# Optimization experiments

Hardware: AMD Instinct MI355X
Metric: run time of the kernel (lower is better)

Reference implementation:

```python
import jax, jax.numpy as jnp
import numpy as np

ALPHA, BETA, GAMMA = 67.0, 3.0, 1.0  # DenseCRFParams3d defaults
NUM_ITERATIONS = 5


def _gauss_kernel(feats):
    # feats: (F, N) scaled features; returns (N, N) kernel exp(-0.5*||f_i-f_j||^2)
    sq = jnp.sum(feats * feats, axis=0)
    d2 = sq[:, None] + sq[None, :] - 2.0 * (feats.T @ feats)
    return jnp.exp(-0.5 * jnp.maximum(d2, 0.0))


def _filter(K, q_ln):
    # K: (N, N) symmetric Gaussian kernel; q_ln: (L, N)
    # normalized Gaussian filtering (splat/blur/slice with slice normalization)
    out = q_ln @ K  # (L, N); K symmetric
    norm = jnp.sum(K, axis=0)  # K @ ones
    return out / norm[None, :]


def setup_inputs() -> dict:
    key = jax.random.key(0)
    k1, k2 = jax.random.split(key)
    L, C, D, W, H = 21, 3, 16, 16, 16
    image = jax.random.uniform(k1, (1, C, D, W, H), dtype=jnp.float32)
    logits = jax.random.normal(k2, (1, L, D, W, H), dtype=jnp.float32)
    spatial_ker_weights = 3.0 * jnp.eye(L, dtype=jnp.float32)
    bilateral_ker_weights = 5.0 * jnp.eye(L, dtype=jnp.float32)
    compatibility_matrix = jnp.eye(L, dtype=jnp.float32)
    return {
        "image": image,
        "logits": logits,
        "spatial_ker_weights": spatial_ker_weights,
        "bilateral_ker_weights": bilateral_ker_weights,
        "compatibility_matrix": compatibility_matrix,
    }


def reference(image, logits, spatial_ker_weights, bilateral_ker_weights, compatibility_matrix):
    img = image[0]            # (C, D, W, H)
    unary = logits[0]         # (L, D, W, H)
    C, D, W, H = img.shape
    L = unary.shape[0]
    N = D * W * H

    # voxel coordinates (3, N)
    zz, yy, xx = jnp.meshgrid(jnp.arange(D), jnp.arange(W), jnp.arange(H), indexing="ij")
    pos = jnp.stack([zz, yy, xx]).reshape(3, N).astype(jnp.float32)

    # kernels are fixed across iterations -> build once
    K_sp = _gauss_kernel(pos / GAMMA)                                   # spatial kernel
    feats_bi = jnp.concatenate([pos / ALPHA, img.reshape(C, N) / BETA], axis=0)
    K_bi = _gauss_kernel(feats_bi)                                      # bilateral kernel

    cur = unary
    for _ in range(NUM_ITERATIONS):
        q = jax.nn.softmax(cur, axis=0).reshape(L, N)
        spatial_out = spatial_ker_weights @ _filter(K_sp, q)
        bilateral_out = bilateral_ker_weights @ _filter(K_bi, q)
        msg = compatibility_matrix @ (spatial_out + bilateral_out)
        cur = msg.reshape(L, D, W, H) + unary
    return cur[None]  # (1, L, D, W, H)
```

## Files before the change

kernel.cpp:

```cpp
#include <hip/hip_runtime.h>

#define L 21
#define NVOX 4096
#define ITERS 5
#define NU 210
#define UPAD 224
#define VPB 16
#define NSPLIT 16
#define USPL 14

__global__ __launch_bounds__(256) void phase_ab(
    const float* __restrict__ img, const float* __restrict__ logits,
    const float* __restrict__ Wsp, const float* __restrict__ Wbi,
    const float* __restrict__ Wc,
    float* __restrict__ Phi, float* __restrict__ nsp, float* __restrict__ q,
    float* __restrict__ cu, float* __restrict__ W1, float* __restrict__ W2,
    float* __restrict__ A2)
{
    const int tid = threadIdx.x;
    const int bid = blockIdx.x;
    if (bid < 64) {
        int lane = tid & 63, w = tid >> 6;
        int i = bid * 64 + lane;
        int z = i >> 8, yy = (i >> 4) & 15, xx = i & 15;
        const float ia = 1.0f / 67.0f, ib = 1.0f / 3.0f;
        float f[6];
        f[0] = (float)z * ia; f[1] = (float)yy * ia; f[2] = (float)xx * ia;
        f[3] = img[i] * ib; f[4] = img[NVOX + i] * ib; f[5] = img[2 * NVOX + i] * ib;
        float p[6][5];
#pragma unroll
        for (int c = 0; c < 6; c++) {
            p[c][0] = 1.f;
#pragma unroll
            for (int k = 1; k < 5; k++) p[c][k] = p[c][k - 1] * f[c];
        }
        float hsv = 0.5f * (f[0]*f[0] + f[1]*f[1] + f[2]*f[2] +
                            f[3]*f[3] + f[4]*f[4] + f[5]*f[5]);
        float e0 = __expf(-hsv);
        int ulo = w * 56, uhi = ulo + 56;
        int u = 0;
        for (int a0 = 0; a0 <= 4; a0++)
        for (int a1 = 0; a1 <= 4 - a0; a1++)
        for (int a2 = 0; a2 <= 4 - a0 - a1; a2++)
        for (int a3 = 0; a3 <= 4 - a0 - a1 - a2; a3++)
        for (int a4 = 0; a4 <= 4 - a0 - a1 - a2 - a3; a4++)
        for (int a5 = 0; a5 <= 4 - a0 - a1 - a2 - a3 - a4; a5++) {
            if (u >= ulo && u < uhi)
                Phi[(size_t)u * NVOX + i] =
                    e0 * p[0][a0] * p[1][a1] * p[2][a2] * p[3][a3] * p[4][a4] * p[5][a5];
            u++;
        }
        if (w == 3)
            for (int uz = NU; uz < UPAD; uz++) Phi[(size_t)uz * NVOX + i] = 0.f;
        if (w == 0) {
            float hz = 0.f, hy = 0.f, hx = 0.f;
            for (int t = 0; t < 16; t++) {
                float dz = (float)(z - t), dy = (float)(yy - t), dx = (float)(xx - t);
                hz += __expf(-0.5f * dz * dz);
                hy += __expf(-0.5f * dy * dy);
                hx += __expf(-0.5f * dx * dx);
            }
            nsp[i] = hz * hy * hx;
        }
        if (w == 1) {
            float vals[L]; float mx = -1e30f;
#pragma unroll
            for (int l = 0; l < L; l++) { vals[l] = logits[l * NVOX + i]; mx = fmaxf(mx, vals[l]); }
            float sum = 0.f;
#pragma unroll
            for (int l = 0; l < L; l++) { vals[l] = __expf(vals[l] - mx); sum += vals[l]; }
            float inv = 1.f / sum;
#pragma unroll
            for (int l = 0; l < L; l++) q[l * NVOX + i] = vals[l] * inv;
        }
    } else if (bid == 64) {
        for (int e = tid; e < L * L; e += 256) {
            int r = e / L, c = e % L;
            float s1 = 0.f, s2 = 0.f;
            for (int k = 0; k < L; k++) {
                float wc = Wc[r * L + k];
                s1 = fmaf(wc, Wsp[k * L + c], s1);
                s2 = fmaf(wc, Wbi[k * L + c], s2);
            }
            W1[e] = s1; W2[e] = s2;
        }
    } else if (bid == 65) {
        const float invf[5] = {1.f, 1.f, 0.5f, 1.f / 6.f, 1.f / 24.f};
        float mine = 0.f;
        int v = 0;
        for (int a0 = 0; a0 <= 4; a0++)
        for (int a1 = 0; a1 <= 4 - a0; a1++)
        for (int a2 = 0; a2 <= 4 - a0 - a1; a2++)
        for (int a3 = 0; a3 <= 4 - a0 - a1 - a2; a3++)
        for (int a4 = 0; a4 <= 4 - a0 - a1 - a2 - a3; a4++)
        for (int a5 = 0; a5 <= 4 - a0 - a1 - a2 - a3 - a4; a5++) {
            if (v == tid)
                mine = invf[a0] * invf[a1] * invf[a2] * invf[a3] * invf[a4] * invf[a5];
            v++;
        }
        cu[tid] = mine;
    } else {
        for (int e = tid; e < 2 * 22 * UPAD; e += 256) A2[e] = 0.f;
    }
}

__global__ __launch_bounds__(1024) void phase_p2(
    const float* __restrict__ Phi, const float* __restrict__ q,
    const float* __restrict__ cu, const float* __restrict__ W2,
    float* __restrict__ A2cur, float* __restrict__ spv)
{
    __shared__ float buf[NVOX];
    __shared__ float tmp[NVOX];
    __shared__ float g[16];
    const int tid = threadIdx.x;
    const int bid = blockIdx.x;
    if (bid < NU) {
        int lane = tid & 63, w = tid >> 4 >> 2;
        int i0 = w * 256;
        float4 p = ((const float4*)(Phi + (size_t)bid * NVOX + i0))[lane];
        float acc[22];
        acc[21] = p.x + p.y + p.z + p.w;
#pragma unroll
        for (int m = 0; m < L; m++) {
            float4 qv = ((const float4*)(q + m * NVOX + i0))[lane];
            acc[m] = fmaf(qv.x, p.x, fmaf(qv.y, p.y,
                     fmaf(qv.z, p.z, qv.w * p.w)));
        }
#pragma unroll
        for (int off = 32; off >= 1; off >>= 1)
#pragma unroll
            for (int m = 0; m < 22; m++)
                acc[m] += __shfl_xor(acc[m], off);
        if (lane < 22) {
            float val;
            if (lane < L) {
                float dot = 0.f;
#pragma unroll
                for (int m = 0; m < L; m++)
                    dot = fmaf(W2[lane * L + m], acc[m], dot);
                val = cu[bid] * dot;
            } else {
                val = cu[bid] * acc[21];
            }
            atomicAdd(&A2cur[lane * UPAD + bid], val);
        }
    } else {
        int l = bid - NU;
        if (tid < 16) g[tid] = __expf(-0.5f * (float)(tid * tid));
        for (int k = 0; k < 4; k++)
            buf[tid + 1024 * k] = q[l * NVOX + tid + 1024 * k];
        __syncthreads();
        for (int k = 0; k < 4; k++) {
            int idx = tid + 1024 * k;
            int x = idx & 15, base = idx & ~15;
            float ssum = 0.f;
#pragma unroll
            for (int t = 0; t < 16; t++) {
                int d = x - t; d = d < 0 ? -d : d;
                ssum += g[d] * buf[base + t];
            }
            tmp[idx] = ssum;
        }
        __syncthreads();
        for (int k = 0; k < 4; k++) {
            int idx = tid + 1024 * k;
            int y = (idx >> 4) & 15, base = idx & ~(15 << 4);
            float ssum = 0.f;
#pragma unroll
            for (int t = 0; t < 16; t++) {
                int d = y - t; d = d < 0 ? -d : d;
                ssum += g[d] * tmp[base + (t << 4)];
            }
            buf[idx] = ssum;
        }
        __syncthreads();
        for (int k = 0; k < 4; k++) {
            int idx = tid + 1024 * k;
            int z = idx >> 8, base = idx & 255;
            float ssum = 0.f;
#pragma unroll
            for (int t = 0; t < 16; t++) {
                int d = z - t; d = d < 0 ? -d : d;
                ssum += g[d] * buf[base + (t << 8)];
            }
            spv[l * NVOX + idx] = ssum;
        }
    }
}

__global__ __launch_bounds__(256) void phase_p3(
    const float* __restrict__ Phi, const float* __restrict__ A2cur,
    float* __restrict__ A2next, const float* __restrict__ spv,
    const float* __restrict__ nsp, const float* __restrict__ W1,
    const float* __restrict__ logits, float* __restrict__ q,
    float* __restrict__ out, int last)
{
    __shared__ float sA[L * UPAD];
    __shared__ float sN[UPAD];
    __shared__ float red[22][NSPLIT][VPB];
    __shared__ float sw1[L * L];
    __shared__ float sspn[VPB][22];
    __shared__ float scur[VPB][22];
    const int tid = threadIdx.x;
    const int bid = blockIdx.x;
    const int v = tid & (VPB - 1);
    const int s = tid >> 4;
    const int i16 = bid * VPB + v;

    {
        int e = bid * 256 + tid;
        if (e < 22 * UPAD) A2next[e] = 0.f;
    }
    for (int e = tid; e < L * UPAD; e += 256) sA[e] = A2cur[e];
    for (int e = tid; e < UPAD; e += 256) sN[e] = A2cur[L * UPAD + e];
    for (int e = tid; e < L * L; e += 256) sw1[e] = W1[e];
    {
        float rsp = 1.f / nsp[i16];
        for (int m = s; m < L; m += NSPLIT)
            sspn[v][m] = spv[m * NVOX + i16] * rsp;
    }
    __syncthreads();
    float acc[L], accN = 0.f;
#pragma unroll
    for (int m = 0; m < L; m++) acc[m] = 0.f;
    int u0 = s * USPL;
    for (int uu = 0; uu < USPL; uu++) {
        float p = Phi[(size_t)(u0 + uu) * NVOX + i16];
#pragma unroll
        for (int m = 0; m < L; m++)
            acc[m] = fmaf(sA[m * UPAD + u0 + uu], p, acc[m]);
        accN = fmaf(sN[u0 + uu], p, accN);
    }
#pragma unroll
    for (int m = 0; m < L; m++) red[m][s][v] = acc[m];
    red[21][s][v] = accN;
    __syncthreads();
    float b21 = 0.f;
#pragma unroll
    for (int ss = 0; ss < NSPLIT; ss++) b21 += red[21][ss][v];
    float rbi = 1.f / b21;
    for (int l = s; l < L; l += NSPLIT) {
        float bl = 0.f;
#pragma unroll
        for (int ss = 0; ss < NSPLIT; ss++) bl += red[l][ss][v];
        float r = bl * rbi;
#pragma unroll
        for (int m = 0; m < L; m++)
            r = fmaf(sw1[l * L + m], sspn[v][m], r);
        r += logits[l * NVOX + i16];
        scur[v][l] = r;
        if (last) out[l * NVOX + i16] = r;
    }
    __syncthreads();
    if (!last && tid < VPB) {
        int i = bid * VPB + tid;
        float vals[L]; float mx = -1e30f;
#pragma unroll
        for (int l = 0; l < L; l++) { vals[l] = scur[tid][l]; mx = fmaxf(mx, vals[l]); }
        float sum = 0.f;
#pragma unroll
        for (int l = 0; l < L; l++) { vals[l] = __expf(vals[l] - mx); sum += vals[l]; }
        float inv = 1.f / sum;
#pragma unroll
        for (int l = 0; l < L; l++) q[l * NVOX + i] = vals[l] * inv;
    }
}

extern "C" void kernel_launch(void* const* d_in, const int* in_sizes, int n_in,
                              void* d_out, int out_size, void* d_ws, size_t ws_size,
                              hipStream_t stream) {
    const float* image  = (const float*)d_in[0];
    const float* logits = (const float*)d_in[1];
    const float* Wsp    = (const float*)d_in[2];
    const float* Wbi    = (const float*)d_in[3];
    const float* Wc     = (const float*)d_in[4];
    float* out = (float*)d_out;

    char* ws = (char*)d_ws;
    float* Phi   = (float*)ws; ws += (size_t)UPAD * NVOX * sizeof(float);
    float* nsp   = (float*)ws; ws += (size_t)NVOX * sizeof(float);
    float* q     = (float*)ws; ws += (size_t)L * NVOX * sizeof(float);
    float* spv   = (float*)ws; ws += (size_t)L * NVOX * sizeof(float);
    float* A2    = (float*)ws; ws += (size_t)2 * 22 * UPAD * sizeof(float);
    float* cu    = (float*)ws; ws += (size_t)256 * sizeof(float);
    float* W1    = (float*)ws; ws += (size_t)L * L * sizeof(float);
    float* W2    = (float*)ws; ws += (size_t)L * L * sizeof(float);

    phase_ab<<<67, 256, 0, stream>>>(image, logits, Wsp, Wbi, Wc,
                                     Phi, nsp, q, cu, W1, W2, A2);
    for (int it = 0; it < ITERS; it++) {
        float* A2cur  = A2 + (it & 1) * 22 * UPAD;
        float* A2next = A2 + ((it + 1) & 1) * 22 * UPAD;
        phase_p2<<<NU + L, 1024, 0, stream>>>(Phi, q, cu, W2, A2cur, spv);
        phase_p3<<<256, 256, 0, stream>>>(Phi, A2cur, A2next, spv, nsp,
                                          W1, logits, q, out,
                                          it == ITERS - 1 ? 1 : 0);
    }
}
```

Measured before the change: 160.8 us.

## Process four feature rows per block and truncate spatial blur to radius four

The projection phase now assigns four feature rows to each block, with each wave covering 1024 voxels over four float4 steps. This cuts the grid from 210 to 56 projection blocks and reduces shuffle reductions and atomics per row. The separable spatial blur drops taps beyond distance four and uses constant weights in registers instead of shared memory, which changes results slightly (dropped weights are below about 4e-6). Shared-memory staging of A2 in phase_p3 is switched to float4 loads.

```diff
diff --git a/kernel.cpp b/kernel.cpp
--- a/kernel.cpp
+++ b/kernel.cpp
@@ -8,6 +8,7 @@
 #define VPB 16
 #define NSPLIT 16
 #define USPL 14
+#define NG1B 56
 
 __global__ __launch_bounds__(256) void phase_ab(
     const float* __restrict__ img, const float* __restrict__ logits,
@@ -111,20 +112,29 @@
 {
     __shared__ float buf[NVOX];
     __shared__ float tmp[NVOX];
-    __shared__ float g[16];
     const int tid = threadIdx.x;
     const int bid = blockIdx.x;
-    if (bid < NU) {
-        int lane = tid & 63, w = tid >> 4 >> 2;
-        int i0 = w * 256;
-        float4 p = ((const float4*)(Phi + (size_t)bid * NVOX + i0))[lane];
+    const float garr[5] = {1.0f, 0.60653066f, 0.13533528f,
+                           0.011108997f, 3.3546263e-4f};
+    if (bid < NG1B) {
+        const int lane = tid & 63, wv = tid >> 6;
+        const int u = bid * 4 + (wv >> 2);
+        const int i0 = (wv & 3) * 1024;
         float acc[22];
-        acc[21] = p.x + p.y + p.z + p.w;
-#pragma unroll
-        for (int m = 0; m < L; m++) {
-            float4 qv = ((const float4*)(q + m * NVOX + i0))[lane];
-            acc[m] = fmaf(qv.x, p.x, fmaf(qv.y, p.y,
-                     fmaf(qv.z, p.z, qv.w * p.w)));
+#pragma unroll
+        for (int m = 0; m < 22; m++) acc[m] = 0.f;
+        const float4* ph = (const float4*)(Phi + (size_t)u * NVOX + i0);
+#pragma unroll
+        for (int rep = 0; rep < 4; rep++) {
+            int ii = rep * 64 + lane;
+            float4 pv = ph[ii];
+            acc[21] += pv.x + pv.y + pv.z + pv.w;
+#pragma unroll
+            for (int m = 0; m < L; m++) {
+                float4 qv = ((const float4*)(q + m * NVOX + i0))[ii];
+                acc[m] = fmaf(qv.x, pv.x, fmaf(qv.y, pv.y,
+                         fmaf(qv.z, pv.z, fmaf(qv.w, pv.w, acc[m]))));
+            }
         }
 #pragma unroll
         for (int off = 32; off >= 1; off >>= 1)
@@ -138,15 +148,14 @@
 #pragma unroll
                 for (int m = 0; m < L; m++)
                     dot = fmaf(W2[lane * L + m], acc[m], dot);
-                val = cu[bid] * dot;
+                val = cu[u] * dot;
             } else {
-                val = cu[bid] * acc[21];
-            }
-            atomicAdd(&A2cur[lane * UPAD + bid], val);
+                val = cu[u] * acc[21];
+            }
+            atomicAdd(&A2cur[lane * UPAD + u], val);
         }
     } else {
-        int l = bid - NU;
-        if (tid < 16) g[tid] = __expf(-0.5f * (float)(tid * tid));
+        int l = bid - NG1B;
         for (int k = 0; k < 4; k++)
             buf[tid + 1024 * k] = q[l * NVOX + tid + 1024 * k];
         __syncthreads();
@@ -155,9 +164,10 @@
             int x = idx & 15, base = idx & ~15;
             float ssum = 0.f;
 #pragma unroll
-            for (int t = 0; t < 16; t++) {
-                int d = x - t; d = d < 0 ? -d : d;
-                ssum += g[d] * buf[base + t];
+            for (int dt = -4; dt <= 4; dt++) {
+                int t = x + dt;
+                int ad = dt < 0 ? -dt : dt;
+                if (t >= 0 && t < 16) ssum = fmaf(garr[ad], buf[base + t], ssum);
             }
             tmp[idx] = ssum;
         }
@@ -167,9 +177,10 @@
             int y = (idx >> 4) & 15, base = idx & ~(15 << 4);
             float ssum = 0.f;
 #pragma unroll
-            for (int t = 0; t < 16; t++) {
-                int d = y - t; d = d < 0 ? -d : d;
-                ssum += g[d] * tmp[base + (t << 4)];
+            for (int dt = -4; dt <= 4; dt++) {
+                int t = y + dt;
+                int ad = dt < 0 ? -dt : dt;
+                if (t >= 0 && t < 16) ssum = fmaf(garr[ad], tmp[base + (t << 4)], ssum);
             }
             buf[idx] = ssum;
         }
@@ -179,9 +190,10 @@
             int z = idx >> 8, base = idx & 255;
             float ssum = 0.f;
 #pragma unroll
-            for (int t = 0; t < 16; t++) {
-                int d = z - t; d = d < 0 ? -d : d;
-                ssum += g[d] * buf[base + (t << 8)];
+            for (int dt = -4; dt <= 4; dt++) {
+                int t = z + dt;
+                int ad = dt < 0 ? -dt : dt;
+                if (t >= 0 && t < 16) ssum = fmaf(garr[ad], buf[base + (t << 8)], ssum);
             }
             spv[l * NVOX + idx] = ssum;
         }
@@ -195,8 +207,8 @@
     const float* __restrict__ logits, float* __restrict__ q,
     float* __restrict__ out, int last)
 {
-    __shared__ float sA[L * UPAD];
-    __shared__ float sN[UPAD];
+    __shared__ __align__(16) float sA[L * UPAD];
+    __shared__ __align__(16) float sN[UPAD];
     __shared__ float red[22][NSPLIT][VPB];
     __shared__ float sw1[L * L];
     __shared__ float sspn[VPB][22];
@@ -211,8 +223,10 @@
         int e = bid * 256 + tid;
         if (e < 22 * UPAD) A2next[e] = 0.f;
     }
-    for (int e = tid; e < L * UPAD; e += 256) sA[e] = A2cur[e];
-    for (int e = tid; e < UPAD; e += 256) sN[e] = A2cur[L * UPAD + e];
+    for (int e = tid; e < (L * UPAD) / 4; e += 256)
+        ((float4*)sA)[e] = ((const float4*)A2cur)[e];
+    if (tid < UPAD / 4)
+        ((float4*)sN)[tid] = ((const float4*)(A2cur + L * UPAD))[tid];
     for (int e = tid; e < L * L; e += 256) sw1[e] = W1[e];
     {
         float rsp = 1.f / nsp[i16];
@@ -291,7 +305,7 @@
     for (int it = 0; it < ITERS; it++) {
         float* A2cur  = A2 + (it & 1) * 22 * UPAD;
         float* A2next = A2 + ((it + 1) & 1) * 22 * UPAD;
-        phase_p2<<<NU + L, 1024, 0, stream>>>(Phi, q, cu, W2, A2cur, spv);
+        phase_p2<<<NG1B + L, 1024, 0, stream>>>(Phi, q, cu, W2, A2cur, spv);
         phase_p3<<<256, 256, 0, stream>>>(Phi, A2cur, A2next, spv, nsp,
                                           W1, logits, q, out,
                                           it == ITERS - 1 ? 1 : 0);
```

Result: slower. 233.0 us (+44.8%).
